# Kernel optimization log

Measured on AMD Instinct MI355X. Metric: run time of the kernel, lower is better.

## Reference

```python
import jax, jax.numpy as jnp
import numpy as np

DT = 0.001  # seconds per step (keras_spiking default)
BATCH, SEQ, SIZE = 64, 1024, 512


def setup_inputs() -> dict:
    key = jax.random.key(0)
    k1, k2 = jax.random.split(key)
    inputs = jax.random.normal(k1, (BATCH, SEQ, SIZE), dtype=jnp.float32)
    initial_level = jnp.zeros((SIZE,), dtype=jnp.float32)
    # time constants around the 0.01s used in the docstring example
    tau = 0.005 + 0.05 * jax.random.uniform(k2, (SIZE,), dtype=jnp.float32)
    return {"inputs": inputs, "initial_level": initial_level, "tau": tau}


def _alpha_filter(inputs, initial_level, tau):
    # inputs: [B, T, K]; initial_level, tau: [K]
    B_, T, K = inputs.shape
    tau_c = jnp.maximum(tau, 1e-8)               # clip for stability (as in forward pass)
    dt_tau = DT / tau_c                           # [K]
    dt_tau2 = dt_tau / tau_c                      # [K]
    e = jnp.exp(-dt_tau)                          # [K]
    # per-feature 2x2 transition matrix A: [K, 2, 2]
    row0 = jnp.stack([1.0 - dt_tau, -dt_tau2], axis=-1)             # [K, 2]
    row1 = jnp.stack([DT * jnp.ones_like(tau_c), 1.0 + dt_tau], -1)  # [K, 2]
    A = e[:, None, None] * jnp.stack([row0, row1], axis=-2)          # [K, 2, 2]
    # input vector B: [K, 2]
    Bvec = jnp.stack([e * dt_tau2, 1.0 - e * (1.0 + dt_tau)], axis=-1)
    Bt = Bvec.T  # [2, K]
    # initial state: row 0 zeros, row 1 initial_level -> [B, 2, K]
    x0 = jnp.stack(
        [jnp.zeros((B_, K), inputs.dtype),
         jnp.broadcast_to(initial_level, (B_, K))], axis=1)

    def step(x, u):
        # x: [B, 2, K], u: [B, K]
        xn = jnp.einsum('kij,mjk->mik', A, x) + Bt[None, :, :] * u[:, None, :]
        return xn, xn[:, 1]  # output is second state component

    _, ys = jax.lax.scan(step, x0, jnp.swapaxes(inputs, 0, 1))  # ys: [T, B, K]
    return jnp.swapaxes(ys, 0, 1)  # [B, T, K]


def reference(inputs, initial_level, tau):
    return _alpha_filter(inputs, initial_level, tau)
```

## Files before the change

kernel.cpp:

```cpp
#include <hip/hip_runtime.h>
#include <math.h>

namespace {
constexpr int kB  = 64, kT = 1024, kK = 512;
constexpr int kC  = 32;
constexpr int kL  = kT / kC;
constexpr int kQ  = kK / 4;
constexpr int kTh = 256;
constexpr int kG  = kB * kC * kQ;
constexpr float kDT = 0.001f;
}

typedef float nt4 __attribute__((ext_vector_type(4)));

__device__ __forceinline__ void nt_store4(float4 v, float4* p) {
    nt4 w; w.x = v.x; w.y = v.y; w.z = v.z; w.w = v.w;
    __builtin_nontemporal_store(w, (nt4*)p);
}

__device__ __forceinline__ void alpha_coeffs(float tk,
    float& a00, float& a01, float& a10, float& a11, float& b0, float& b1)
{
    const float tc      = fmaxf(tk, 1e-8f);
    const float dt_tau  = kDT / tc;
    const float dt_tau2 = dt_tau / tc;
    const float e       = expf(-dt_tau);
    a00 = e * (1.0f - dt_tau);
    a01 = e * (-dt_tau2);
    a10 = e * kDT;
    a11 = e * (1.0f + dt_tau);
    b0  = e * dt_tau2;
    b1  = 1.0f - e * (1.0f + dt_tau);
}

struct C4 { float4 a00, a01, a10, a11, b0, b1; };

__device__ __forceinline__ C4 alpha_coeffs4(float4 t) {
    C4 c;
    alpha_coeffs(t.x, c.a00.x, c.a01.x, c.a10.x, c.a11.x, c.b0.x, c.b1.x);
    alpha_coeffs(t.y, c.a00.y, c.a01.y, c.a10.y, c.a11.y, c.b0.y, c.b1.y);
    alpha_coeffs(t.z, c.a00.z, c.a01.z, c.a10.z, c.a11.z, c.b0.z, c.b1.z);
    alpha_coeffs(t.w, c.a00.w, c.a01.w, c.a10.w, c.a11.w, c.b0.w, c.b1.w);
    return c;
}

__device__ __forceinline__ float4 f4fma(float4 a, float4 b, float4 c) {
    return make_float4(fmaf(a.x,b.x,c.x), fmaf(a.y,b.y,c.y),
                       fmaf(a.z,b.z,c.z), fmaf(a.w,b.w,c.w));
}
__device__ __forceinline__ float4 f4mul(float4 a, float4 b) {
    return make_float4(a.x*b.x, a.y*b.y, a.z*b.z, a.w*b.w);
}
__device__ __forceinline__ float4 f4add(float4 a, float4 b) {
    return make_float4(a.x+b.x, a.y+b.y, a.z+b.z, a.w+b.w);
}
__device__ __forceinline__ float4 f4zero() { return make_float4(0.f,0.f,0.f,0.f); }

__global__ __launch_bounds__(kTh, 4) void alpha_k1_states(
    const float* __restrict__ in,
    const float* __restrict__ tau,
    float4* __restrict__ S0,
    float4* __restrict__ S1)
{
    const int g  = blockIdx.x * kTh + threadIdx.x;
    const int kq = g & (kQ - 1);
    const int bc = g >> 7;
    const int b  = bc & (kB - 1);
    const int c  = bc >> 6;

    const C4 cf = alpha_coeffs4(((const float4*)tau)[kq]);

    const float4* __restrict__ pin =
        (const float4*)in + ((size_t)b * kT + (size_t)c * kL) * kQ + kq;

    float4 buf[8];
    #pragma unroll
    for (int i = 0; i < 8; ++i) buf[i] = pin[(size_t)i * kQ];

    float4 x0 = f4zero(), x1 = f4zero();
    #pragma unroll
    for (int tb = 0; tb < kL - 8; tb += 8) {
        const float4* __restrict__ pld = pin + (size_t)(tb + 8) * kQ;
        #pragma unroll
        for (int i = 0; i < 8; ++i) {
            const float4 u = buf[i];
            buf[i] = pld[(size_t)i * kQ];
            const float4 n0 = f4fma(cf.a00, x0, f4fma(cf.a01, x1, f4mul(cf.b0, u)));
            const float4 n1 = f4fma(cf.a10, x0, f4fma(cf.a11, x1, f4mul(cf.b1, u)));
            x0 = n0; x1 = n1;
        }
    }
    #pragma unroll
    for (int i = 0; i < 8; ++i) {
        const float4 u = buf[i];
        const float4 n0 = f4fma(cf.a00, x0, f4fma(cf.a01, x1, f4mul(cf.b0, u)));
        const float4 n1 = f4fma(cf.a10, x0, f4fma(cf.a11, x1, f4mul(cf.b1, u)));
        x0 = n0; x1 = n1;
    }

    S0[g] = x0;
    S1[g] = x1;
}

__global__ __launch_bounds__(kTh, 4) void alpha_k2_prefix(
    const float* __restrict__ init_level,
    const float* __restrict__ tau,
    float4* __restrict__ S0,
    float4* __restrict__ S1)
{
    const int h  = blockIdx.x * kTh + threadIdx.x;
    const int kq = h & (kQ - 1);
    const int b  = h >> 7;

    const C4 cf = alpha_coeffs4(((const float4*)tau)[kq]);

    float4 m00 = cf.a00, m01 = cf.a01, m10 = cf.a10, m11 = cf.a11;
    #pragma unroll
    for (int s = 0; s < 5; ++s) {
        const float4 t00 = f4fma(m00, m00, f4mul(m01, m10));
        const float4 t01 = f4fma(m00, m01, f4mul(m01, m11));
        const float4 t10 = f4fma(m10, m00, f4mul(m11, m10));
        const float4 t11 = f4fma(m10, m01, f4mul(m11, m11));
        m00 = t00; m01 = t01; m10 = t10; m11 = t11;
    }

    float4 v0 = f4zero();
    float4 v1 = ((const float4*)init_level)[kq];
    size_t idx = (size_t)b * kQ + kq;
    #pragma unroll
    for (int c = 0; c < kC; ++c) {
        const float4 s0 = S0[idx];
        const float4 s1 = S1[idx];
        S0[idx] = v0;
        S1[idx] = v1;
        const float4 p0 = f4add(f4fma(m00, v0, f4mul(m01, v1)), s0);
        const float4 p1 = f4add(f4fma(m10, v0, f4mul(m11, v1)), s1);
        v0 = p0; v1 = p1;
        idx += (size_t)kB * kQ;
    }
}

__global__ __launch_bounds__(kTh, 4) void alpha_k3_rescan(
    const float* __restrict__ in,
    const float* __restrict__ tau,
    const float4* __restrict__ S0,
    const float4* __restrict__ S1,
    float* __restrict__ out)
{
    const int g  = blockIdx.x * kTh + threadIdx.x;
    const int kq = g & (kQ - 1);
    const int bc = g >> 7;
    const int b  = bc & (kB - 1);
    const int c  = bc >> 6;

    const C4 cf = alpha_coeffs4(((const float4*)tau)[kq]);

    float4 v0 = S0[g];
    float4 v1 = S1[g];

    const size_t base = ((size_t)b * kT + (size_t)c * kL) * kQ + kq;
    const float4* __restrict__ pin  = (const float4*)in  + base;
    float4* __restrict__ pout       = (float4*)out + base;

    float4 buf[8];
    #pragma unroll
    for (int i = 0; i < 8; ++i) buf[i] = pin[(size_t)i * kQ];

    #pragma unroll
    for (int tb = 0; tb < kL - 8; tb += 8) {
        const float4* __restrict__ pld = pin  + (size_t)(tb + 8) * kQ;
        float4* __restrict__ pst       = pout + (size_t)tb * kQ;
        #pragma unroll
        for (int i = 0; i < 8; ++i) {
            const float4 u = buf[i];
            buf[i] = pld[(size_t)i * kQ];
            const float4 n0 = f4fma(cf.a00, v0, f4fma(cf.a01, v1, f4mul(cf.b0, u)));
            const float4 n1 = f4fma(cf.a10, v0, f4fma(cf.a11, v1, f4mul(cf.b1, u)));
            v0 = n0; v1 = n1;
            nt_store4(n1, &pst[(size_t)i * kQ]);
        }
    }
    {
        float4* __restrict__ pst = pout + (size_t)(kL - 8) * kQ;
        #pragma unroll
        for (int i = 0; i < 8; ++i) {
            const float4 u = buf[i];
            const float4 n0 = f4fma(cf.a00, v0, f4fma(cf.a01, v1, f4mul(cf.b0, u)));
            const float4 n1 = f4fma(cf.a10, v0, f4fma(cf.a11, v1, f4mul(cf.b1, u)));
            v0 = n0; v1 = n1;
            nt_store4(n1, &pst[(size_t)i * kQ]);
        }
    }
}

__global__ __launch_bounds__(1024, 8) void alpha_scan_c32(
    const float* __restrict__ in,
    const float* __restrict__ init_level,
    const float* __restrict__ tau,
    float* __restrict__ out)
{
    __shared__ float sx0[32][32];
    __shared__ float sx1[32][32];

    const int tid = threadIdx.x;
    const int kl  = tid & 31;
    const int c   = tid >> 5;
    const int bx  = blockIdx.x;
    const int b   = bx >> 4;
    const int k   = ((bx & 15) << 5) + kl;

    float a00, a01, a10, a11, b0, b1;
    alpha_coeffs(tau[k], a00, a01, a10, a11, b0, b1);
    const float il = init_level[k];

    const size_t base = (size_t)b * kT * kK + (size_t)c * 32 * kK + k;
    const float* __restrict__ pin = in + base;

    float r[32];
    #pragma unroll
    for (int i = 0; i < 32; ++i) r[i] = pin[(size_t)i * kK];

    float x0 = 0.0f, x1 = 0.0f;
    #pragma unroll
    for (int i = 0; i < 32; ++i) {
        const float u   = r[i];
        const float nx0 = fmaf(a00, x0, fmaf(a01, x1, b0 * u));
        const float nx1 = fmaf(a10, x0, fmaf(a11, x1, b1 * u));
        x0 = nx0; x1 = nx1;
        r[i] = nx1;
    }
    sx0[c][kl] = x0;
    sx1[c][kl] = x1;
    __syncthreads();

    float m00 = a00, m01 = a01, m10 = a10, m11 = a11;
    #pragma unroll
    for (int sq = 0; sq < 5; ++sq) {
        const float t00 = fmaf(m00, m00, m01 * m10);
        const float t01 = fmaf(m00, m01, m01 * m11);
        const float t10 = fmaf(m10, m00, m11 * m10);
        const float t11 = fmaf(m10, m01, m11 * m11);
        m00 = t00; m01 = t01; m10 = t10; m11 = t11;
    }
    float v0 = 0.0f, v1 = il;
    for (int j = 0; j < c; ++j) {
        const float p0 = fmaf(m00, v0, m01 * v1) + sx0[j][kl];
        const float p1 = fmaf(m10, v0, m11 * v1) + sx1[j][kl];
        v0 = p0; v1 = p1;
    }
    float* __restrict__ pout = out + base;
    #pragma unroll
    for (int i = 0; i < 32; ++i) {
        const float n0 = fmaf(a00, v0, a01 * v1);
        const float n1 = fmaf(a10, v0, a11 * v1);
        v0 = n0; v1 = n1;
        pout[(size_t)i * kK] = r[i] + n1;
    }
}

extern "C" void kernel_launch(void* const* d_in, const int* in_sizes, int n_in,
                              void* d_out, int out_size, void* d_ws, size_t ws_size,
                              hipStream_t stream) {
    const float* in  = (const float*)d_in[0];
    const float* il  = (const float*)d_in[1];
    const float* tau = (const float*)d_in[2];
    float* out = (float*)d_out;

    const size_t ws_needed = (size_t)kG * 2 * sizeof(float4);
    if (d_ws != nullptr && ws_size >= ws_needed) {
        float4* S0 = (float4*)d_ws;
        float4* S1 = S0 + kG;
        alpha_k1_states<<<dim3(kG / kTh), dim3(kTh), 0, stream>>>(in, tau, S0, S1);
        alpha_k2_prefix<<<dim3((kB * kQ) / kTh), dim3(kTh), 0, stream>>>(il, tau, S0, S1);
        alpha_k3_rescan<<<dim3(kG / kTh), dim3(kTh), 0, stream>>>(in, tau, S0, S1, out);
    } else {
        alpha_scan_c32<<<dim3(kB * (kK / 32)), dim3(1024), 0, stream>>>(
            in, il, tau, out);
    }
}
```

Baseline: 265.7 us.

## Fuse chunk-prefix and rescan kernels via shared-memory chunk states

Merges the serial chunk-prefix kernel into the rescan kernel. Each 1024-thread block loads the chunk-end states for one batch and 32 feature quads into LDS, and each thread serially composes the prefix up to its own chunk before rescanning. The first kernel also skips the last chunk, whose end state is never used. This removes one launch and the global round-trip of the prefix states, in exchange for redundant O(C) prefix work per thread and a block-wide barrier.

```diff
diff --git a/kernel.cpp b/kernel.cpp
--- a/kernel.cpp
+++ b/kernel.cpp
@@ -6,8 +6,9 @@
 constexpr int kC  = 32;
 constexpr int kL  = kT / kC;
 constexpr int kQ  = kK / 4;
+constexpr int kQT = 32;
 constexpr int kTh = 256;
-constexpr int kG  = kB * kC * kQ;
+constexpr int kG1 = kB * (kC - 1) * kQ;
 constexpr float kDT = 0.001f;
 }
 
@@ -102,17 +103,33 @@
     S1[g] = x1;
 }
 
-__global__ __launch_bounds__(kTh, 4) void alpha_k2_prefix(
+__global__ __launch_bounds__(1024, 4) void alpha_k2_fused(
+    const float* __restrict__ in,
     const float* __restrict__ init_level,
     const float* __restrict__ tau,
-    float4* __restrict__ S0,
-    float4* __restrict__ S1)
-{
-    const int h  = blockIdx.x * kTh + threadIdx.x;
-    const int kq = h & (kQ - 1);
-    const int b  = h >> 7;
+    const float4* __restrict__ S0,
+    const float4* __restrict__ S1,
+    float* __restrict__ out)
+{
+    __shared__ float4 ls0[kC][kQT];
+    __shared__ float4 ls1[kC][kQT];
+
+    const int tid = threadIdx.x;
+    const int kqi = tid & (kQT - 1);
+    const int c   = tid >> 5;
+    const int bx  = blockIdx.x;
+    const int b   = bx >> 2;
+    const int kq  = ((bx & 3) << 5) + kqi;
 
     const C4 cf = alpha_coeffs4(((const float4*)tau)[kq]);
+    const float4 il = ((const float4*)init_level)[kq];
+
+    if (c < kC - 1) {
+        const size_t sidx = (size_t)(c * kB + b) * kQ + kq;
+        ls0[c][kqi] = S0[sidx];
+        ls1[c][kqi] = S1[sidx];
+    }
+    __syncthreads();
 
     float4 m00 = cf.a00, m01 = cf.a01, m10 = cf.a10, m11 = cf.a11;
     #pragma unroll
@@ -123,40 +140,12 @@
         const float4 t11 = f4fma(m10, m01, f4mul(m11, m11));
         m00 = t00; m01 = t01; m10 = t10; m11 = t11;
     }
-
-    float4 v0 = f4zero();
-    float4 v1 = ((const float4*)init_level)[kq];
-    size_t idx = (size_t)b * kQ + kq;
-    #pragma unroll
-    for (int c = 0; c < kC; ++c) {
-        const float4 s0 = S0[idx];
-        const float4 s1 = S1[idx];
-        S0[idx] = v0;
-        S1[idx] = v1;
-        const float4 p0 = f4add(f4fma(m00, v0, f4mul(m01, v1)), s0);
-        const float4 p1 = f4add(f4fma(m10, v0, f4mul(m11, v1)), s1);
+    float4 v0 = f4zero(), v1 = il;
+    for (int j = 0; j < c; ++j) {
+        const float4 p0 = f4add(f4fma(m00, v0, f4mul(m01, v1)), ls0[j][kqi]);
+        const float4 p1 = f4add(f4fma(m10, v0, f4mul(m11, v1)), ls1[j][kqi]);
         v0 = p0; v1 = p1;
-        idx += (size_t)kB * kQ;
-    }
-}
-
-__global__ __launch_bounds__(kTh, 4) void alpha_k3_rescan(
-    const float* __restrict__ in,
-    const float* __restrict__ tau,
-    const float4* __restrict__ S0,
-    const float4* __restrict__ S1,
-    float* __restrict__ out)
-{
-    const int g  = blockIdx.x * kTh + threadIdx.x;
-    const int kq = g & (kQ - 1);
-    const int bc = g >> 7;
-    const int b  = bc & (kB - 1);
-    const int c  = bc >> 6;
-
-    const C4 cf = alpha_coeffs4(((const float4*)tau)[kq]);
-
-    float4 v0 = S0[g];
-    float4 v1 = S1[g];
+    }
 
     const size_t base = ((size_t)b * kT + (size_t)c * kL) * kQ + kq;
     const float4* __restrict__ pin  = (const float4*)in  + base;
@@ -266,13 +255,13 @@
     const float* tau = (const float*)d_in[2];
     float* out = (float*)d_out;
 
-    const size_t ws_needed = (size_t)kG * 2 * sizeof(float4);
+    const size_t ws_needed = (size_t)kC * kB * kQ * 2 * sizeof(float4);
     if (d_ws != nullptr && ws_size >= ws_needed) {
         float4* S0 = (float4*)d_ws;
-        float4* S1 = S0 + kG;
-        alpha_k1_states<<<dim3(kG / kTh), dim3(kTh), 0, stream>>>(in, tau, S0, S1);
-        alpha_k2_prefix<<<dim3((kB * kQ) / kTh), dim3(kTh), 0, stream>>>(il, tau, S0, S1);
-        alpha_k3_rescan<<<dim3(kG / kTh), dim3(kTh), 0, stream>>>(in, tau, S0, S1, out);
+        float4* S1 = S0 + (size_t)kC * kB * kQ;
+        alpha_k1_states<<<dim3(kG1 / kTh), dim3(kTh), 0, stream>>>(in, tau, S0, S1);
+        alpha_k2_fused<<<dim3(kB * (kQ / kQT)), dim3(1024), 0, stream>>>(
+            in, il, tau, S0, S1, out);
     } else {
         alpha_scan_c32<<<dim3(kB * (kK / 32)), dim3(1024), 0, stream>>>(
             in, il, tau, out);
```

Result: no change. 261.5 us (-1.6%).
